# Kernel tuning notes

Measured on AMD Instinct MI355X. Metric: run time of the kernel, lower is better.

## Reference

```python
import jax, jax.numpy as jnp
import numpy as np

F_N = 100000   # binary factors
V_N = 30000    # variables
E_N = 1000000  # GAT edges
DEG = 3        # sources per v2f target
D = 15         # msg_dim / domain size
HID = 60       # in_channels - prefix_dim
IN = 64        # in_channels
OUT = 32       # out_channels
T_N = 2 * F_N          # number of v2f (= f2v) messages
N_N = V_N + 5 * F_N    # GAT nodes


def _gru(x, h, w_ih, w_hh, b_ih, b_hh):
    gi = x @ w_ih.T + b_ih
    gh = h @ w_hh.T + b_hh
    ir, iz, i_n = jnp.split(gi, 3, axis=1)
    hr, hz, h_n = jnp.split(gh, 3, axis=1)
    r = jax.nn.sigmoid(ir + hr)
    z = jax.nn.sigmoid(iz + hz)
    n = jnp.tanh(i_n + r * h_n)
    return (1.0 - z) * n + z * h


def _gat(x, src, dst, W, a_src, a_dst, bias, heads, out_dim, concat):
    n = x.shape[0]
    h = (x @ W).reshape(n, heads, out_dim)
    e = jax.nn.leaky_relu((h * a_src).sum(-1)[src] + (h * a_dst).sum(-1)[dst], 0.2)
    emax = jax.ops.segment_max(e, dst, num_segments=n)
    w = jnp.exp(e - emax[dst])
    den = jax.ops.segment_sum(w, dst, num_segments=n)
    alpha = w / (den[dst] + 1e-16)
    out = jax.ops.segment_sum(h[src] * alpha[:, :, None], dst, num_segments=n)
    out = out.reshape(n, heads * out_dim) if concat else out.mean(axis=1)
    return out + bias


def _attn(q, k, Wq, Wk, Ws, b):
    return jax.nn.sigmoid(jnp.concatenate([q @ Wq.T, k @ Wk.T], axis=1) @ Ws.T + b)


def _forward(msgs, cost_tensors, func_embed, v2f_hidden, f2v_hidden, embed_table,
             w_ih1, w_hh1, b_ih1, b_hh1, w_ih2, w_hh2, b_ih2, b_hh2,
             W1, as1, ad1, bb1, W2, as2, ad2, bb2, W3, as3, ad3, bb3,
             W4, as4, ad4, bb4, Wq, Wk, Ws, bs_att,
             edge_index, var_colors,
             msg_rv2f_idxes, msg_cv2f_idxes, msg_f2rv_idxes, msg_f2cv_idxes,
             msg_src_idxes, msg_trg_idxes, msg_f2v_per_v_idxes,
             embed_trg_idxes, embed_src_idxes, v2f_scatter_idxes,
             f2v_per_v_scatter_idxes, f_batch, rv_idxes, cv_idxes):
    Fn = cost_tensors.shape[0]
    T = msg_trg_idxes.shape[0]
    # ---- min-plus BP factor updates ----
    m_rv2f = msgs[msg_rv2f_idxes]
    m_cv2f = msgs[msg_cv2f_idxes]
    m_f2rv = jnp.min(cost_tensors + m_cv2f[:, None, :], axis=2)
    m_f2cv = jnp.min(cost_tensors + m_rv2f[:, :, None], axis=1)
    msgs = msgs.at[msg_f2rv_idxes].set(m_f2rv).at[msg_f2cv_idxes].set(m_f2cv)
    # ---- GRU state updates (inputs detached as in source) ----
    v2f_h = _gru(jax.lax.stop_gradient(jnp.concatenate([m_rv2f, m_cv2f], axis=0)),
                 v2f_hidden, w_ih1, w_hh1, b_ih1, b_hh1)
    f2v_h = _gru(jax.lax.stop_gradient(jnp.concatenate([m_f2rv, m_f2cv], axis=0)),
                 f2v_hidden, w_ih2, w_hh2, b_ih2, b_hh2)
    # ---- node features with 4-dim one-hot type prefixes (VAR_ID/V2F_ID/F2V_ID) ----
    ve = embed_table[var_colors]
    def pref(t, v):
        p = jnp.zeros((v.shape[0], 4), v.dtype).at[:, t].set(1.0)
        return jnp.concatenate([p, v], axis=1)
    x = jnp.concatenate([pref(0, ve), func_embed, pref(1, v2f_h), pref(2, f2v_h)], axis=0)
    # ---- GAT stack with self loops ----
    n = x.shape[0]
    loops = jnp.arange(n, dtype=edge_index.dtype)
    src = jnp.concatenate([edge_index[0], loops])
    dst = jnp.concatenate([edge_index[1], loops])
    x = jax.nn.leaky_relu(_gat(x, src, dst, W1, as1, ad1, bb1, 4, 8, True), 0.01)
    x = jax.nn.leaky_relu(_gat(x, src, dst, W2, as2, ad2, bb2, 4, 8, True), 0.01)
    x = jax.nn.leaky_relu(_gat(x, src, dst, W3, as3, ad3, bb3, 4, 8, True), 0.01)
    x = jax.nn.leaky_relu(_gat(x, src, dst, W4, as4, ad4, bb4, 4, OUT, False), 0.01)
    # ---- scatter-softmax attention aggregation over v2f targets ----
    msg_src = msgs[msg_src_idxes]
    msg_trg = msgs[msg_trg_idxes]
    e_src = x[embed_src_idxes]
    e_trg = x[embed_trg_idxes]
    e_trg_rep = e_trg[v2f_scatter_idxes]  # == repeat_interleave by degree (idxes sorted)
    deg = jax.ops.segment_sum(jnp.ones((v2f_scatter_idxes.shape[0],), x.dtype),
                              v2f_scatter_idxes, num_segments=T)
    scores = _attn(e_trg_rep, e_src, Wq, Wk, Ws, bs_att)   # [TD, 1]
    trg_scores = _attn(e_trg, e_trg, Wq, Wk, Ws, bs_att)   # [T, 1]
    smax = jax.ops.segment_max(scores, v2f_scatter_idxes, num_segments=T)
    w = jnp.exp(scores - smax[v2f_scatter_idxes])
    den = jax.ops.segment_sum(w, v2f_scatter_idxes, num_segments=T)
    aw = w / den[v2f_scatter_idxes]
    weighted = jax.ops.segment_sum(msg_src[:, :, None] * aw[:, None, :],
                                   v2f_scatter_idxes, num_segments=T)  # [T, D, 1]
    weighted = weighted.mean(axis=-1) * deg[:, None]
    mean_scores = jax.ops.segment_sum(scores, v2f_scatter_idxes, num_segments=T) / deg[:, None]
    damped = jax.nn.softmax(jnp.stack([mean_scores, trg_scores], axis=1), axis=1)  # [T, 2, 1]
    v2f = weighted[:, :, None] * damped[:, 0][:, None, :] + msg_trg[:, :, None] * damped[:, 1][:, None, :]
    v2f = v2f.mean(axis=-1)
    v2f = v2f - v2f.min(axis=1, keepdims=True)
    msgs = msgs.at[msg_trg_idxes].set(v2f)
    # ---- beliefs, entropy, loss ----
    belief = jax.ops.segment_sum(msgs[msg_f2v_per_v_idxes], f2v_per_v_scatter_idxes,
                                 num_segments=V_N)
    dist = jax.nn.softmax(-belief, axis=1)
    ent = -(dist * jnp.log2(dist + 1e-6)).sum(axis=1).mean()
    drv = dist[rv_idxes]
    dcv = dist[cv_idxes]
    per_f = jnp.einsum('fi,fij,fj->f', drv, cost_tensors, dcv)
    loss = jax.ops.segment_sum(per_f, f_batch, num_segments=1).mean() + 0.1 * ent
    vr = jnp.argmax(drv, axis=1)
    vc = jnp.argmax(dcv, axis=1)
    cost = cost_tensors[jnp.arange(Fn), vr, vc]
    cost_mean = jax.ops.segment_sum(cost, f_batch, num_segments=1).mean()
    return loss, cost_mean


def setup_inputs():
    key = jax.random.key(0)
    ks = jax.random.split(key, 24)
    f32 = jnp.float32
    s = 0.1
    inp = {}
    inp['msgs'] = jax.random.normal(ks[0], (4 * F_N, D), f32)
    inp['cost_tensors'] = jax.random.uniform(ks[1], (F_N, D, D), f32)
    inp['func_embed'] = jax.random.normal(ks[2], (F_N, IN), f32) * s
    inp['v2f_hidden'] = jax.random.normal(ks[3], (T_N, HID), f32) * s
    inp['f2v_hidden'] = jax.random.normal(ks[4], (T_N, HID), f32) * s
    inp['embed_table'] = jax.random.normal(ks[5], (100, HID), f32) * s
    inp['w_ih1'] = jax.random.normal(ks[6], (3 * HID, D), f32) * s
    inp['w_hh1'] = jax.random.normal(ks[7], (3 * HID, HID), f32) * s
    inp['b_ih1'] = jnp.zeros((3 * HID,), f32)
    inp['b_hh1'] = jnp.zeros((3 * HID,), f32)
    inp['w_ih2'] = jax.random.normal(ks[8], (3 * HID, D), f32) * s
    inp['w_hh2'] = jax.random.normal(ks[9], (3 * HID, HID), f32) * s
    inp['b_ih2'] = jnp.zeros((3 * HID,), f32)
    inp['b_hh2'] = jnp.zeros((3 * HID,), f32)
    inp['W1'] = jax.random.normal(ks[10], (IN, 32), f32) * s
    inp['as1'] = jax.random.normal(ks[11], (4, 8), f32) * s
    inp['ad1'] = jax.random.normal(ks[12], (4, 8), f32) * s
    inp['bb1'] = jnp.zeros((32,), f32)
    inp['W2'] = jax.random.normal(ks[13], (32, 32), f32) * s
    inp['as2'] = jax.random.normal(ks[14], (4, 8), f32) * s
    inp['ad2'] = jax.random.normal(ks[15], (4, 8), f32) * s
    inp['bb2'] = jnp.zeros((32,), f32)
    inp['W3'] = jax.random.normal(ks[16], (32, 32), f32) * s
    inp['as3'] = jax.random.normal(ks[17], (4, 8), f32) * s
    inp['ad3'] = jax.random.normal(ks[18], (4, 8), f32) * s
    inp['bb3'] = jnp.zeros((32,), f32)
    inp['W4'] = jax.random.normal(ks[19], (32, 4 * OUT), f32) * s
    inp['as4'] = jax.random.normal(ks[20], (4, OUT), f32) * s
    inp['ad4'] = jax.random.normal(ks[21], (4, OUT), f32) * s
    inp['bb4'] = jnp.zeros((OUT,), f32)
    inp['Wq'] = jax.random.normal(ks[22], (OUT, OUT), f32) * s
    inp['Wk'] = jax.random.normal(ks[23], (OUT, OUT), f32) * s
    k2 = jax.random.split(jax.random.fold_in(key, 1), 8)
    inp['Ws'] = jax.random.normal(k2[0], (1, 2 * OUT), f32) * s
    inp['bs_att'] = jnp.zeros((1,), f32)
    inp['edge_index'] = jax.random.randint(k2[1], (2, E_N), 0, N_N, jnp.int32)
    inp['var_colors'] = jax.random.randint(k2[2], (V_N,), 0, 100, jnp.int32)
    inp['msg_rv2f_idxes'] = jnp.arange(0, F_N, dtype=jnp.int32)
    inp['msg_cv2f_idxes'] = jnp.arange(F_N, 2 * F_N, dtype=jnp.int32)
    inp['msg_f2rv_idxes'] = jnp.arange(2 * F_N, 3 * F_N, dtype=jnp.int32)
    inp['msg_f2cv_idxes'] = jnp.arange(3 * F_N, 4 * F_N, dtype=jnp.int32)
    inp['msg_src_idxes'] = jax.random.randint(k2[3], (T_N * DEG,), 2 * F_N, 4 * F_N, jnp.int32)
    inp['msg_trg_idxes'] = jnp.arange(0, T_N, dtype=jnp.int32)
    inp['msg_f2v_per_v_idxes'] = jnp.arange(2 * F_N, 4 * F_N, dtype=jnp.int32)
    inp['embed_trg_idxes'] = V_N + F_N + inp['msg_trg_idxes']
    inp['embed_src_idxes'] = V_N + F_N + inp['msg_src_idxes']
    inp['v2f_scatter_idxes'] = jnp.repeat(jnp.arange(T_N, dtype=jnp.int32), DEG)
    inp['f2v_per_v_scatter_idxes'] = jnp.concatenate([
        jnp.arange(V_N, dtype=jnp.int32),
        jax.random.randint(k2[4], (T_N - V_N,), 0, V_N, jnp.int32)])
    inp['f_batch'] = jnp.zeros((F_N,), jnp.int32)
    inp['rv_idxes'] = jax.random.randint(k2[5], (F_N,), 0, V_N, jnp.int32)
    inp['cv_idxes'] = jax.random.randint(k2[6], (F_N,), 0, V_N, jnp.int32)
    return inp


def reference(msgs, cost_tensors, func_embed, v2f_hidden, f2v_hidden, embed_table,
              w_ih1, w_hh1, b_ih1, b_hh1, w_ih2, w_hh2, b_ih2, b_hh2,
              W1, as1, ad1, bb1, W2, as2, ad2, bb2, W3, as3, ad3, bb3,
              W4, as4, ad4, bb4, Wq, Wk, Ws, bs_att,
              edge_index, var_colors,
              msg_rv2f_idxes, msg_cv2f_idxes, msg_f2rv_idxes, msg_f2cv_idxes,
              msg_src_idxes, msg_trg_idxes, msg_f2v_per_v_idxes,
              embed_trg_idxes, embed_src_idxes, v2f_scatter_idxes,
              f2v_per_v_scatter_idxes, f_batch, rv_idxes, cv_idxes):
    return _forward(msgs, cost_tensors, func_embed, v2f_hidden, f2v_hidden, embed_table,
                    w_ih1, w_hh1, b_ih1, b_hh1, w_ih2, w_hh2, b_ih2, b_hh2,
                    W1, as1, ad1, bb1, W2, as2, ad2, bb2, W3, as3, ad3, bb3,
                    W4, as4, ad4, bb4, Wq, Wk, Ws, bs_att,
                    edge_index, var_colors,
                    msg_rv2f_idxes, msg_cv2f_idxes, msg_f2rv_idxes, msg_f2cv_idxes,
                    msg_src_idxes, msg_trg_idxes, msg_f2v_per_v_idxes,
                    embed_trg_idxes, embed_src_idxes, v2f_scatter_idxes,
                    f2v_per_v_scatter_idxes, f_batch, rv_idxes, cv_idxes)
```

## Files before the change

kernel.cpp:

```cpp
#include <hip/hip_runtime.h>

#define F_N 100000
#define V_N 30000
#define DD 15
#define DP 16
#define TILE 225
#define T_N (2 * F_N)
#define NSLOT 256
#define MPB 16
#define CAP 32

static const size_t M_OFF     = 0;
static const size_t DIST_OFF  = 3200000;
static const size_t CNT_OFF   = 3680000;
static const size_t TLIST_OFF = 3710048;
static const size_t AMAX_OFF  = 4670048;
static const size_t SLOTP_OFF = 4700064;
static const size_t SLOTC_OFF = 4700320;
static const size_t SLOTE_OFF = 4700576;

__global__ void k_init(int* __restrict__ cnt, float* __restrict__ slots) {
    int i = blockIdx.x * blockDim.x + threadIdx.x;
    if (i < V_N) cnt[i] = 0;
    if (i < 3 * NSLOT) slots[i] = 0.0f;
}

__global__ void k_place(const int* __restrict__ scat,
                        int* __restrict__ cnt,
                        int* __restrict__ tlist) {
    int t = blockIdx.x * blockDim.x + threadIdx.x;
    if (t < T_N) {
        int v = scat[t];
        int pos = atomicAdd(&cnt[v], 1);
        if (pos < CAP) tlist[v * CAP + pos] = t;
    }
}

__global__ __launch_bounds__(256) void k_minplus(
        const float* __restrict__ msgs,
        const float* __restrict__ cost,
        float* __restrict__ m) {
    __shared__ __align__(16) float tile[MPB * TILE];
    __shared__ float mlds[2 * MPB * DD];
    int f0  = blockIdx.x * MPB;
    int tid = threadIdx.x;

    const float4* src4 = reinterpret_cast<const float4*>(cost + (size_t)f0 * TILE);
    float4* dst4 = reinterpret_cast<float4*>(tile);
#pragma unroll
    for (int e4 = tid; e4 < MPB * TILE / 4; e4 += 256)
        dst4[e4] = src4[e4];
    for (int e = tid; e < 2 * MPB * DD; e += 256)
        mlds[e] = (e < MPB * DD) ? msgs[(size_t)f0 * DD + e]
                                 : msgs[(size_t)(F_N + f0) * DD + (e - MPB * DD)];
    __syncthreads();

    int r = tid & 31;
#pragma unroll
    for (int h = 0; h < 2; ++h) {
        int q = (tid >> 5) + 8 * h;
        if (r < 30) {
            bool is_row = (r < DD);
            int i = is_row ? r : (r - DD);
            int f = f0 + q;
            const float* mb = is_row ? &mlds[MPB * DD + q * DD] : &mlds[q * DD];
            const float* Cf = &tile[q * TILE];
            float mn = 1e30f;
#pragma unroll
            for (int k = 0; k < DD; ++k) {
                int a = is_row ? (i * DD + k) : (k * DD + i);
                mn = fminf(mn, Cf[a] + mb[k]);
            }
            size_t t = is_row ? (size_t)f : (size_t)(F_N + f);
            m[t * DP + i] = mn;
        }
    }
}

__global__ __launch_bounds__(256) void k_gather_softmax(
        const float* __restrict__ m,
        const int* __restrict__ cnt,
        const int* __restrict__ tlist,
        float* __restrict__ dist,
        int*   __restrict__ amax,
        float* __restrict__ slotE) {
    int gid = blockIdx.x * 256 + threadIdx.x;
    int v = gid >> 4;
    int k = gid & 15;
    bool act = (v < V_N) && (k < DD);
    float b0 = 0.0f, b1 = 0.0f;
    if (v < V_N) {
        int n = cnt[v];
        if (n > CAP) n = CAP;
        int n1 = (n < 16) ? n : 16;
        int tl  = (k < n)       ? tlist[v * CAP + k]      : 0;
        int tl2 = (k + 16 < n)  ? tlist[v * CAP + k + 16] : 0;
        int i = 0;
        for (; i + 1 < n1; i += 2) {
            int ta = __shfl(tl, i, 16);
            int tb = __shfl(tl, i + 1, 16);
            if (k < DD) {
                b0 += m[(size_t)ta * DP + k];
                b1 += m[(size_t)tb * DP + k];
            }
        }
        if (i < n1) {
            int ta = __shfl(tl, i, 16);
            if (k < DD) b0 += m[(size_t)ta * DP + k];
        }
        for (int j = 16; j < n; ++j) {
            int ta = __shfl(tl2, j - 16, 16);
            if (k < DD) b1 += m[(size_t)ta * DP + k];
        }
    }
    float b = b0 + b1;
    float bm = act ? b : 1e30f;
#pragma unroll
    for (int off = 1; off < 16; off <<= 1) bm = fminf(bm, __shfl_xor(bm, off, 16));
    float e = act ? expf(bm - b) : 0.0f;
    float den = e;
#pragma unroll
    for (int off = 1; off < 16; off <<= 1) den += __shfl_xor(den, off, 16);
    float dk = e / den;
    float entp = 0.0f;
    if (act) {
        dist[(size_t)v * DP + k] = dk;
        entp = -dk * log2f(dk + 1e-6f);
    }
    float av = act ? dk : -1.0f;
    int   ai = k;
#pragma unroll
    for (int off = 1; off < 16; off <<= 1) {
        float ov = __shfl_xor(av, off, 16);
        int   oi = __shfl_xor(ai, off, 16);
        if (ov > av || (ov == av && oi < ai)) { av = ov; ai = oi; }
    }
    if (k == 0 && v < V_N) amax[v] = ai;
#pragma unroll
    for (int off = 32; off > 0; off >>= 1) entp += __shfl_down(entp, off, 64);
    __shared__ float sE[4];
    if ((threadIdx.x & 63) == 0) sE[threadIdx.x >> 6] = entp;
    __syncthreads();
    if (threadIdx.x == 0)
        atomicAdd(&slotE[blockIdx.x & (NSLOT - 1)], sE[0] + sE[1] + sE[2] + sE[3]);
}

__global__ __launch_bounds__(256) void k_factor_loss(
        const float* __restrict__ cost,
        const float* __restrict__ dist,
        const int*   __restrict__ amax,
        const int*   __restrict__ rv_idx,
        const int*   __restrict__ cv_idx,
        float* __restrict__ slotP,
        float* __restrict__ slotC) {
    int gtid = blockIdx.x * 256 + threadIdx.x;
    int f    = gtid >> 6;
    int lane = threadIdx.x & 63;
    float s = 0.0f, c = 0.0f;
    if (f < F_N) {
        int rv = rv_idx[f], cv = cv_idx[f];
        float drv = dist[(size_t)rv * DP + (lane & 15)];
        float dcv = dist[(size_t)cv * DP + (lane & 15)];
        const float* Cf = cost + (size_t)f * TILE;
#pragma unroll
        for (int t = 0; t < 4; ++t) {
            int e = lane + t * 64;
            if (e < TILE) {
                int i = e / DD;
                int j = e - i * DD;
                s += __shfl(drv, i, 64) * Cf[e] * __shfl(dcv, j, 64);
            }
        }
        if (lane == 0) c = Cf[amax[rv] * DD + amax[cv]];
    }
#pragma unroll
    for (int off = 32; off > 0; off >>= 1) s += __shfl_down(s, off, 64);
    __shared__ float sP[4], sC[4];
    int w = threadIdx.x >> 6;
    if (lane == 0) { sP[w] = s; sC[w] = c; }
    __syncthreads();
    if (threadIdx.x == 0) {
        float tp = sP[0] + sP[1] + sP[2] + sP[3];
        float tc = sC[0] + sC[1] + sC[2] + sC[3];
        int slot = blockIdx.x & (NSLOT - 1);
        atomicAdd(&slotP[slot], tp);
        atomicAdd(&slotC[slot], tc);
    }
}

__global__ void k_final(const float* __restrict__ slotP,
                        const float* __restrict__ slotC,
                        const float* __restrict__ slotE,
                        float* __restrict__ out) {
    int t = threadIdx.x;
    float p = slotP[t], c = slotC[t], g = slotE[t];
#pragma unroll
    for (int off = 32; off > 0; off >>= 1) {
        p += __shfl_down(p, off, 64);
        c += __shfl_down(c, off, 64);
        g += __shfl_down(g, off, 64);
    }
    __shared__ float sp[4], sc[4], se[4];
    if ((t & 63) == 0) { sp[t >> 6] = p; sc[t >> 6] = c; se[t >> 6] = g; }
    __syncthreads();
    if (t == 0) {
        float tp = sp[0] + sp[1] + sp[2] + sp[3];
        float tc = sc[0] + sc[1] + sc[2] + sc[3];
        float te = se[0] + se[1] + se[2] + se[3];
        out[0] = tp + 0.1f * (te / (float)V_N);
        out[1] = tc;
    }
}

extern "C" void kernel_launch(void* const* d_in, const int* in_sizes, int n_in,
                              void* d_out, int out_size, void* d_ws, size_t ws_size,
                              hipStream_t stream) {
    const float* msgs = (const float*)d_in[0];
    const float* cost = (const float*)d_in[1];
    const int* scat   = (const int*)d_in[46];
    const int* rv     = (const int*)d_in[48];
    const int* cv     = (const int*)d_in[49];

    float* ws    = (float*)d_ws;
    float* m     = ws + M_OFF;
    float* dist  = ws + DIST_OFF;
    int*   cnt   = (int*)(ws + CNT_OFF);
    int*   tlist = (int*)(ws + TLIST_OFF);
    int*   amax  = (int*)(ws + AMAX_OFF);
    float* slotP = ws + SLOTP_OFF;
    float* slotC = ws + SLOTC_OFF;
    float* slotE = ws + SLOTE_OFF;
    float* out   = (float*)d_out;

    k_init<<<(V_N + 255) / 256, 256, 0, stream>>>(cnt, slotP);
    k_place<<<(T_N + 255) / 256, 256, 0, stream>>>(scat, cnt, tlist);
    k_minplus<<<F_N / MPB, 256, 0, stream>>>(msgs, cost, m);
    k_gather_softmax<<<(V_N * 16 + 255) / 256, 256, 0, stream>>>(m, cnt, tlist, dist, amax, slotE);
    k_factor_loss<<<(F_N * 64 + 255) / 256, 256, 0, stream>>>(cost, dist, amax, rv, cv, slotP, slotC);
    k_final<<<1, 256, 0, stream>>>(slotP, slotC, slotE, out);
}
```

Before: 98.33 us.

## Compute min-plus factor messages in registers with shuffles instead of LDS tiles

Replaces the shared-memory staging of cost tiles and messages in the min-plus kernel with a register-based scheme. Each 16-lane group owns one factor, and each lane loads one column of the cost matrix. Column minima come from broadcast shuffles, and row minima come from per-row butterfly reductions. This removes the LDS traffic and the barrier, but costs 15×4 shuffle reductions per factor and gives up the fully coalesced float4 loads.

```diff
diff --git a/kernel.cpp b/kernel.cpp
--- a/kernel.cpp
+++ b/kernel.cpp
@@ -7,7 +7,6 @@
 #define TILE 225
 #define T_N (2 * F_N)
 #define NSLOT 256
-#define MPB 16
 #define CAP 32
 
 static const size_t M_OFF     = 0;
@@ -39,41 +38,37 @@
 __global__ __launch_bounds__(256) void k_minplus(
         const float* __restrict__ msgs,
         const float* __restrict__ cost,
-        float* __restrict__ m) {
-    __shared__ __align__(16) float tile[MPB * TILE];
-    __shared__ float mlds[2 * MPB * DD];
-    int f0  = blockIdx.x * MPB;
+        float* __restrict__ m_arr) {
     int tid = threadIdx.x;
-
-    const float4* src4 = reinterpret_cast<const float4*>(cost + (size_t)f0 * TILE);
-    float4* dst4 = reinterpret_cast<float4*>(tile);
-#pragma unroll
-    for (int e4 = tid; e4 < MPB * TILE / 4; e4 += 256)
-        dst4[e4] = src4[e4];
-    for (int e = tid; e < 2 * MPB * DD; e += 256)
-        mlds[e] = (e < MPB * DD) ? msgs[(size_t)f0 * DD + e]
-                                 : msgs[(size_t)(F_N + f0) * DD + (e - MPB * DD)];
-    __syncthreads();
-
-    int r = tid & 31;
-#pragma unroll
-    for (int h = 0; h < 2; ++h) {
-        int q = (tid >> 5) + 8 * h;
-        if (r < 30) {
-            bool is_row = (r < DD);
-            int i = is_row ? r : (r - DD);
-            int f = f0 + q;
-            const float* mb = is_row ? &mlds[MPB * DD + q * DD] : &mlds[q * DD];
-            const float* Cf = &tile[q * TILE];
-            float mn = 1e30f;
-#pragma unroll
-            for (int k = 0; k < DD; ++k) {
-                int a = is_row ? (i * DD + k) : (k * DD + i);
-                mn = fminf(mn, Cf[a] + mb[k]);
-            }
-            size_t t = is_row ? (size_t)f : (size_t)(F_N + f);
-            m[t * DP + i] = mn;
-        }
+    int g   = tid >> 4;
+    int m   = tid & 15;
+    int f   = blockIdx.x * 16 + g;
+    bool act = (m < DD);
+    const float* Cf = cost + (size_t)f * TILE;
+    float v[DD];
+#pragma unroll
+    for (int k = 0; k < DD; ++k)
+        v[k] = act ? Cf[k * DD + m] : 0.0f;
+    float mcv = act ? msgs[(size_t)(F_N + f) * DD + m] : 0.0f;
+    float mrv = act ? msgs[(size_t)f * DD + m]       : 1e30f;
+    float cm = 1e30f;
+#pragma unroll
+    for (int k = 0; k < DD; ++k) {
+        float mrvk = __shfl(mrv, k, 16);
+        cm = fminf(cm, v[k] + mrvk);
+    }
+    float rsel = 0.0f;
+#pragma unroll
+    for (int k = 0; k < DD; ++k) {
+        float t = act ? (v[k] + mcv) : 1e30f;
+#pragma unroll
+        for (int off = 1; off < 16; off <<= 1)
+            t = fminf(t, __shfl_xor(t, off, 16));
+        if (m == k) rsel = t;
+    }
+    if (act) {
+        m_arr[(size_t)f * DP + m]         = rsel;
+        m_arr[(size_t)(F_N + f) * DP + m] = cm;
     }
 }
 
@@ -234,7 +229,7 @@
 
     k_init<<<(V_N + 255) / 256, 256, 0, stream>>>(cnt, slotP);
     k_place<<<(T_N + 255) / 256, 256, 0, stream>>>(scat, cnt, tlist);
-    k_minplus<<<F_N / MPB, 256, 0, stream>>>(msgs, cost, m);
+    k_minplus<<<F_N / 16, 256, 0, stream>>>(msgs, cost, m);
     k_gather_softmax<<<(V_N * 16 + 255) / 256, 256, 0, stream>>>(m, cnt, tlist, dist, amax, slotE);
     k_factor_loss<<<(F_N * 64 + 255) / 256, 256, 0, stream>>>(cost, dist, amax, rv, cv, slotP, slotC);
     k_final<<<1, 256, 0, stream>>>(slotP, slotC, slotE, out);
```

Result: no change. 99.72 us (+1.4%).
